# Kernel optimization log

Hardware: AMD Instinct MI355X
Metric: run time of the kernel (lower is better)

The kernel has to match this reference:

```python
import jax, jax.numpy as jnp
import numpy as np

N_NODES = 100000
N_EDGES = 1600000
B = 16
NMAX = 4096
IN_DIM = 32
H1 = 64      # capacity C
H2 = 128     # 2C
LAT = 64
DEC_H = 128  # 2C
DEC_IN = LAT + 2
FUEL = 5


def _ln(x, g, b):
    m = x.mean(-1, keepdims=True)
    v = x.var(-1, keepdims=True)
    return (x - m) / jnp.sqrt(v + 1e-5) * g + b


def _mlp2(x, wi, bi, g, be, wo, bo):
    # DeepMLP with num_layers=2: in_lin -> LayerNorm -> ReLU -> out_lin
    h = jax.nn.relu(_ln(x @ wi + bi, g, be))
    return h @ wo + bo


def setup_inputs() -> dict:
    key = jax.random.key(0)
    ks = jax.random.split(key, 48)
    d = {}
    d['x'] = jax.random.normal(ks[0], (N_NODES, IN_DIM), jnp.float32)
    d['edge_index'] = jax.random.randint(ks[1], (2, N_EDGES), 0, N_NODES)
    d['batch'] = jnp.sort(jax.random.randint(ks[2], (N_NODES,), 0, B))

    def w(k, shape):
        return (jax.random.normal(k, shape, jnp.float32) * 0.02)

    conv_shapes = {'w1m': (IN_DIM, H1), 'w2m': (H1, H2), 'w3m': (H2, LAT),
                   'w1l': (IN_DIM, H1), 'w2l': (H1, H2), 'w3l': (H2, LAT)}
    i = 3
    for nm, sh in conv_shapes.items():
        d[nm] = w(ks[i], sh); i += 1
        d['b' + nm[1:]] = jnp.zeros((sh[1],), jnp.float32)
    # node_mlp (DeepMLP dec_in->dec_h->dec_h)
    d['nm_wi'] = w(ks[i], (DEC_IN, DEC_H)); i += 1
    d['nm_bi'] = jnp.zeros((DEC_H,), jnp.float32)
    d['nm_g'] = jnp.ones((DEC_H,), jnp.float32)
    d['nm_be'] = jnp.zeros((DEC_H,), jnp.float32)
    d['nm_wo'] = w(ks[i], (DEC_H, DEC_H)); i += 1
    d['nm_bo'] = jnp.zeros((DEC_H,), jnp.float32)
    # heads
    d['ex_w'] = w(ks[i], (DEC_H, 1)); i += 1
    d['ex_b'] = jnp.zeros((1,), jnp.float32)
    d['fu_w'] = w(ks[i], (DEC_H, FUEL)); i += 1
    d['fu_b'] = jnp.zeros((FUEL,), jnp.float32)
    d['al_w'] = w(ks[i], (DEC_H, 1)); i += 1
    d['al_b'] = jnp.zeros((1,), jnp.float32)
    d['sl_w'] = w(ks[i], (DEC_H, 1)); i += 1
    d['sl_b'] = jnp.zeros((1,), jnp.float32)
    # edge_mlp (DeepMLP dec_in->dec_h->8)
    d['em_wi'] = w(ks[i], (DEC_IN, DEC_H)); i += 1
    d['em_bi'] = jnp.zeros((DEC_H,), jnp.float32)
    d['em_g'] = jnp.ones((DEC_H,), jnp.float32)
    d['em_be'] = jnp.zeros((DEC_H,), jnp.float32)
    d['em_wo'] = w(ks[i], (DEC_H, 8)); i += 1
    d['em_bo'] = jnp.zeros((8,), jnp.float32)
    d['pos_all'] = jax.random.normal(ks[i], (NMAX, 2), jnp.float32)
    return d


def reference(x, edge_index, batch,
              w1m, b1m, w2m, b2m, w3m, b3m,
              w1l, b1l, w2l, b2l, w3l, b3l,
              nm_wi, nm_bi, nm_g, nm_be, nm_wo, nm_bo,
              ex_w, ex_b, fu_w, fu_b, al_w, al_b, sl_w, sl_b,
              em_wi, em_bi, em_g, em_be, em_wo, em_bo,
              pos_all):
    # ---- GCN encoder with self-loops and symmetric normalization (PyG GCNConv) ----
    loops = jnp.arange(N_NODES)
    src = jnp.concatenate([edge_index[0], loops])
    dst = jnp.concatenate([edge_index[1], loops])
    deg = jax.ops.segment_sum(jnp.ones(src.shape, jnp.float32), dst, N_NODES)
    dinv = jax.lax.rsqrt(deg)  # deg >= 1 because of self-loops
    norm = (dinv[src] * dinv[dst])[:, None]

    def conv(h, wt, bt):
        hw = h @ wt                                   # [N, F_out]
        return jax.ops.segment_sum(norm * hw[src], dst, N_NODES) + bt

    mu = jax.nn.relu(conv(x, w1m, b1m))
    mu = jax.nn.relu(conv(mu, w2m, b2m))
    mu = jax.nn.relu(conv(mu, w3m, b3m))
    lg = jax.nn.relu(conv(x, w1l, b1l))
    lg = jax.nn.relu(conv(lg, w2l, b2l))
    lg = jax.nn.relu(conv(lg, w3l, b3l))

    cnt = jnp.maximum(jax.ops.segment_sum(jnp.ones((N_NODES,), jnp.float32), batch, B), 1.0)[:, None]
    mu_g = jax.ops.segment_sum(mu, batch, B) / cnt    # global_mean_pool [B, LAT]
    lg_g = jax.ops.segment_sum(lg, batch, B) / cnt

    z = mu_g  # eval-mode latent_sample returns mu

    # ---- decoder ----
    Z = jnp.broadcast_to(z[:, None, :], (B, NMAX, LAT))
    pos = jnp.broadcast_to(pos_all[None], (B, NMAX, 2))
    Zp = jnp.concatenate([Z, pos], -1).reshape(B * NMAX, DEC_IN)
    h = _mlp2(Zp, nm_wi, nm_bi, nm_g, nm_be, nm_wo, nm_bo)
    nodes = (h @ ex_w + ex_b).reshape(B, NMAX, 1)
    fuel = (h @ fu_w + fu_b).reshape(B, NMAX, FUEL)
    alt = (h @ al_w + al_b).reshape(B, NMAX, 1)
    slope = (h @ sl_w + sl_b).reshape(B, NMAX, 1)
    edges = _mlp2(Zp, em_wi, em_bi, em_g, em_be, em_wo, em_bo).reshape(B, NMAX, 8)
    return (nodes, edges, fuel, alt, slope, mu_g, lg_g)
```

## Files before the change

kernel.cpp:

```cpp
#include <hip/hip_runtime.h>
#include <hip/hip_bf16.h>

#define N_NODES 100000
#define N_EDGESC 1600000
#define BATCH_B 16
#define NMAXC 4096
#define LATC 64
#define CAP 64
#define NBINS 391
#define NSB 256
#define EPB ((N_EDGESC + NSB - 1) / NSB)

#define OUT_NODES 0
#define OUT_EDGES 65536
#define OUT_FUEL  589824
#define OUT_ALT   917504
#define OUT_SLOPE 983040
#define OUT_MU    1048576
#define OUT_LG    1049600

typedef float f32x2 __attribute__((ext_vector_type(2)));
typedef float f32x4 __attribute__((ext_vector_type(4)));
typedef short bf16x8 __attribute__((ext_vector_type(8)));
union U4B { uint4 u; bf16x8 b; };

__device__ __forceinline__ unsigned short f2bf(float f) {
    unsigned int u = __float_as_uint(f);
    return (unsigned short)((u + 0x7FFFu + ((u >> 16) & 1u)) >> 16);
}
__device__ __forceinline__ float bf2f(unsigned short h) {
    return __uint_as_float(((unsigned int)h) << 16);
}
__device__ __forceinline__ void f8acc(unsigned int u, float& a0, float& a1, float& a2, float& a3) {
    f32x2 lo = __builtin_amdgcn_cvt_pk_f32_fp8(u, false);
    f32x2 hi = __builtin_amdgcn_cvt_pk_f32_fp8(u, true);
    a0 += lo[0]; a1 += lo[1]; a2 += hi[0]; a3 += hi[1];
}

__global__ void batch_count(const int* __restrict__ batch, int* __restrict__ bcnt, int n) {
    int b = threadIdx.x;
    if (b >= BATCH_B) return;
    int lo = 0, hi = n;
    while (lo < hi) { int mid = (lo + hi) >> 1; if (batch[mid] < b) lo = mid + 1; else hi = mid; }
    int start = lo;
    lo = 0; hi = n;
    while (lo < hi) { int mid = (lo + hi) >> 1; if (batch[mid] <= b) lo = mid + 1; else hi = mid; }
    bcnt[b] = lo - start;
}

__global__ __launch_bounds__(1024) void histA(const int* __restrict__ dst, int* __restrict__ hist) {
    __shared__ int h[NBINS];
    int b = blockIdx.x, t = threadIdx.x;
    for (int i = t; i < NBINS; i += 1024) h[i] = 0;
    __syncthreads();
    int e0 = b * EPB, e1 = min(e0 + EPB, N_EDGESC);
    for (int i = e0 + t; i < e1; i += 1024)
        atomicAdd(&h[dst[i] >> 8], 1);
    __syncthreads();
    for (int i = t; i < NBINS; i += 1024) hist[i * NSB + b] = h[i];
}

__global__ void scanB(int* __restrict__ hist, int* __restrict__ total) {
    __shared__ int sh[NSB];
    int j = blockIdx.x, t = threadIdx.x;
    int v = hist[j * NSB + t];
    sh[t] = v; __syncthreads();
    for (int off = 1; off < NSB; off <<= 1) {
        int u = (t >= off) ? sh[t - off] : 0; __syncthreads();
        sh[t] += u; __syncthreads();
    }
    hist[j * NSB + t] = sh[t] - v;
    if (t == NSB - 1) total[j] = sh[t];
}

__global__ void scanC(const int* __restrict__ total, int* __restrict__ base) {
    __shared__ int sh[512];
    int t = threadIdx.x;
    int v = (t < NBINS) ? total[t] : 0;
    sh[t] = v; __syncthreads();
    for (int off = 1; off < 512; off <<= 1) {
        int u = (t >= off) ? sh[t - off] : 0; __syncthreads();
        sh[t] += u; __syncthreads();
    }
    if (t < NBINS) base[t] = sh[t] - v;
    if (t == NBINS - 1) base[NBINS] = sh[t];
}

__global__ __launch_bounds__(1024) void scatterD(const int* __restrict__ src, const int* __restrict__ dst,
                                                 const int* __restrict__ hist, const int* __restrict__ base,
                                                 unsigned int* __restrict__ sorted) {
    __shared__ int w0[NBINS];
    __shared__ int lc[NBINS];
    int b = blockIdx.x, t = threadIdx.x;
    for (int i = t; i < NBINS; i += 1024) {
        w0[i] = base[i] + hist[i * NSB + b];
        lc[i] = 0;
    }
    __syncthreads();
    int e0 = b * EPB, e1 = min(e0 + EPB, N_EDGESC);
    for (int i = e0 + t; i < e1; i += 1024) {
        int d = dst[i], s = src[i];
        int j = d >> 8;
        int r = atomicAdd(&lc[j], 1);
        sorted[w0[j] + r] = ((unsigned int)s << 8) | (d & 255);
    }
}

__global__ void csr_sorted(const unsigned int* __restrict__ sorted, const int* __restrict__ base,
                           int* __restrict__ adj, int* __restrict__ cnt,
                           float* __restrict__ dinv, int N) {
    __shared__ int lc[256];
    int j = blockIdx.x, t = threadIdx.x;
    lc[t] = 0; __syncthreads();
    int e0 = base[j], e1 = base[j + 1];
    int node0 = j * 256;
    for (int i = e0 + t; i < e1; i += 256) {
        unsigned int pk = sorted[i];
        int d = pk & 255;
        int r = atomicAdd(&lc[d], 1);
        if (r < CAP) adj[(size_t)(node0 + d) * CAP + r] = (int)(pk >> 8);
    }
    __syncthreads();
    int n = node0 + t;
    if (n < N) {
        int c = lc[t];
        cnt[n] = c;
        dinv[n] = rsqrtf((float)(c + 1));
    }
}

__global__ void prescale_x(const float* __restrict__ x, const float* __restrict__ dinv,
                           unsigned int* __restrict__ xs8, int total4) {
    int i4 = blockIdx.x * 256 + threadIdx.x;
    if (i4 < total4) {
        float4 v = *(const float4*)&x[i4 * 4];
        float ds = dinv[i4 >> 3] * 64.f;
        unsigned int r = 0;
        r = __builtin_amdgcn_cvt_pk_fp8_f32(v.x * ds, v.y * ds, r, false);
        r = __builtin_amdgcn_cvt_pk_fp8_f32(v.z * ds, v.w * ds, r, true);
        xs8[i4] = r;
    }
}

__global__ void agg_s32(const unsigned int* __restrict__ xs8, const int* __restrict__ cnt,
                        const int* __restrict__ adj, const float* __restrict__ dinv,
                        float* __restrict__ out, int N) {
    int t = threadIdx.x;
    int sub = t >> 3, f = t & 7;
    int n = blockIdx.x * 32 + sub;
    if (n >= N) return;
    float s0 = 0.f, s1 = 0.f, s2 = 0.f, s3 = 0.f;
    f8acc(xs8[(size_t)n * 8 + f], s0, s1, s2, s3);
    int e1 = min(cnt[n], CAP);
    const int* ap = &adj[(size_t)n * CAP];
    int e = 0;
    for (; e + 4 <= e1; e += 4) {
        int i0 = ap[e], i1 = ap[e + 1], i2 = ap[e + 2], i3 = ap[e + 3];
        unsigned int u0 = xs8[(size_t)i0 * 8 + f];
        unsigned int u1 = xs8[(size_t)i1 * 8 + f];
        unsigned int u2 = xs8[(size_t)i2 * 8 + f];
        unsigned int u3 = xs8[(size_t)i3 * 8 + f];
        f8acc(u0, s0, s1, s2, s3); f8acc(u1, s0, s1, s2, s3);
        f8acc(u2, s0, s1, s2, s3); f8acc(u3, s0, s1, s2, s3);
    }
    for (; e < e1; e++) f8acc(xs8[(size_t)ap[e] * 8 + f], s0, s1, s2, s3);
    float d = dinv[n] * (1.f / 64.f);
    *(float4*)&out[(size_t)n * 32 + f * 4] = make_float4(s0 * d, s1 * d, s2 * d, s3 * d);
}

template <bool BIASRELU, bool OUT8>
__global__ void agg128(const unsigned int* __restrict__ tbl, const int* __restrict__ cnt,
                       const int* __restrict__ adj, const float* __restrict__ dinv,
                       const float* __restrict__ bias, void* __restrict__ outv, int N) {
    int t = threadIdx.x;
    int sub = t >> 5, f = t & 31;
    int n = blockIdx.x * 8 + sub;
    if (n >= N) return;
    float s0 = 0.f, s1 = 0.f, s2 = 0.f, s3 = 0.f;
    f8acc(tbl[(size_t)n * 32 + f], s0, s1, s2, s3);
    int e1 = min(cnt[n], CAP);
    const int* ap = &adj[(size_t)n * CAP];
    int e = 0;
    for (; e + 4 <= e1; e += 4) {
        int i0 = ap[e], i1 = ap[e + 1], i2 = ap[e + 2], i3 = ap[e + 3];
        unsigned int u0 = tbl[(size_t)i0 * 32 + f];
        unsigned int u1 = tbl[(size_t)i1 * 32 + f];
        unsigned int u2 = tbl[(size_t)i2 * 32 + f];
        unsigned int u3 = tbl[(size_t)i3 * 32 + f];
        f8acc(u0, s0, s1, s2, s3); f8acc(u1, s0, s1, s2, s3);
        f8acc(u2, s0, s1, s2, s3); f8acc(u3, s0, s1, s2, s3);
    }
    for (; e < e1; e++) f8acc(tbl[(size_t)ap[e] * 32 + f], s0, s1, s2, s3);
    float d = dinv[n] * (1.f / 32.f);
    float v0 = s0 * d, v1 = s1 * d, v2 = s2 * d, v3 = s3 * d;
    if (BIASRELU) {
        float4 bv = *(const float4*)&bias[4 * f];
        v0 = fmaxf(v0 + bv.x, 0.f); v1 = fmaxf(v1 + bv.y, 0.f);
        v2 = fmaxf(v2 + bv.z, 0.f); v3 = fmaxf(v3 + bv.w, 0.f);
    }
    if (OUT8) {
        unsigned int r = 0;
        r = __builtin_amdgcn_cvt_pk_fp8_f32(v0 * 32.f, v1 * 32.f, r, false);
        r = __builtin_amdgcn_cvt_pk_fp8_f32(v2 * 32.f, v3 * 32.f, r, true);
        ((unsigned int*)outv)[(size_t)n * 32 + f] = r;
    } else {
        ushort4 u;
        u.x = f2bf(v0); u.y = f2bf(v1); u.z = f2bf(v2); u.w = f2bf(v3);
        *(ushort4*)&((unsigned short*)outv)[(size_t)n * 128 + 4 * f] = u;
    }
}

template <int K, int F>
__global__ void wprep(const float* __restrict__ Wa, const float* __restrict__ Wb,
                      unsigned int* __restrict__ wfrag) {
    constexpr int S = K / 32, C = F / 16;
    int lane = threadIdx.x;
    int bc = blockIdx.x;
    int c = bc % C;
    int s = (bc / C) % S;
    int y = bc / (C * S);
    const float* W = (y == 0) ? Wa : Wb;
    int col = c * 16 + (lane & 15);
    int k0 = s * 32 + (lane >> 4) * 8;
    unsigned int q[4];
#pragma unroll
    for (int jj = 0; jj < 4; jj++) {
        float lo = W[(size_t)(k0 + 2 * jj) * F + col];
        float hi = W[(size_t)(k0 + 2 * jj + 1) * F + col];
        q[jj] = (unsigned int)f2bf(lo) | ((unsigned int)f2bf(hi) << 16);
    }
    *(uint4*)&wfrag[((size_t)bc * 64 + lane) * 4] = make_uint4(q[0], q[1], q[2], q[3]);
}

template <int K, int F, int IN_STRIDE, int IN_OFF_Y, int OUT_STRIDE, int OUT_OFF_Y,
          bool BIASRELU, bool SCALE, int INMODE, int OUTMODE>
__global__ __launch_bounds__(256) void mfma_conv(
    const void* __restrict__ inv, const unsigned int* __restrict__ wfrag,
    const float* __restrict__ biasa, const float* __restrict__ biasb,
    const float* __restrict__ dinv, void* __restrict__ outv, int N) {
    constexpr int S = K / 32, C = F / 16;
    constexpr int FP = F + 4;
    __shared__ unsigned short buf[4][16][FP];
    int t = threadIdx.x, lane = t & 63, wave = t >> 6;
    int y = blockIdx.y;
    int n0 = blockIdx.x * 64 + wave * 16;
    const float* bias = (y == 0) ? biasa : biasb;
    const unsigned int* wf = wfrag + (size_t)y * S * C * 64 * 4;

    f32x4 acc[C];
#pragma unroll
    for (int c = 0; c < C; c++) acc[c] = (f32x4)(0.f);

    int arow = n0 + (lane & 15);
    bool aok = arow < N;
#pragma unroll
    for (int s = 0; s < S; s++) {
        U4B af; af.u = make_uint4(0u, 0u, 0u, 0u);
        if (aok) {
            if constexpr (INMODE == 2) {
                uint2 u = *(const uint2*)((const unsigned char*)inv +
                            (size_t)arow * IN_STRIDE + y * IN_OFF_Y + s * 32 + (lane >> 4) * 8);
                f32x2 p0 = __builtin_amdgcn_cvt_pk_f32_fp8(u.x, false);
                f32x2 p1 = __builtin_amdgcn_cvt_pk_f32_fp8(u.x, true);
                f32x2 p2 = __builtin_amdgcn_cvt_pk_f32_fp8(u.y, false);
                f32x2 p3 = __builtin_amdgcn_cvt_pk_f32_fp8(u.y, true);
                af.u.x = (unsigned int)f2bf(p0[0]) | ((unsigned int)f2bf(p0[1]) << 16);
                af.u.y = (unsigned int)f2bf(p1[0]) | ((unsigned int)f2bf(p1[1]) << 16);
                af.u.z = (unsigned int)f2bf(p2[0]) | ((unsigned int)f2bf(p2[1]) << 16);
                af.u.w = (unsigned int)f2bf(p3[0]) | ((unsigned int)f2bf(p3[1]) << 16);
            } else if constexpr (INMODE == 1) {
                af.u = *(const uint4*)((const unsigned short*)inv +
                            (size_t)arow * IN_STRIDE + y * IN_OFF_Y + s * 32 + (lane >> 4) * 8);
            } else {
                const float* ap = (const float*)inv + (size_t)arow * IN_STRIDE + y * IN_OFF_Y
                                  + s * 32 + (lane >> 4) * 8;
                float4 v0 = *(const float4*)ap;
                float4 v1 = *(const float4*)(ap + 4);
                af.u.x = (unsigned int)f2bf(v0.x) | ((unsigned int)f2bf(v0.y) << 16);
                af.u.y = (unsigned int)f2bf(v0.z) | ((unsigned int)f2bf(v0.w) << 16);
                af.u.z = (unsigned int)f2bf(v1.x) | ((unsigned int)f2bf(v1.y) << 16);
                af.u.w = (unsigned int)f2bf(v1.z) | ((unsigned int)f2bf(v1.w) << 16);
            }
        }
#pragma unroll
        for (int c = 0; c < C; c++) {
            U4B wb;
            wb.u = *(const uint4*)&wf[((size_t)(s * C + c) * 64 + lane) * 4];
            acc[c] = __builtin_amdgcn_mfma_f32_16x16x32_bf16(af.b, wb.b, acc[c], 0, 0, 0);
        }
    }

    constexpr float ISC = (INMODE == 2) ? (1.f / 32.f) : 1.f;
#pragma unroll
    for (int c = 0; c < C; c++) {
        int col = c * 16 + (lane & 15);
        float bv = BIASRELU ? bias[col] : 0.f;
#pragma unroll
        for (int r = 0; r < 4; r++) {
            int row = (lane >> 4) * 4 + r;
            int n = n0 + row;
            float v = acc[c][r] * ISC;
            if (BIASRELU) v = fmaxf(v + bv, 0.f);
            if (SCALE) v *= dinv[min(n, N - 1)];
            buf[wave][row][col] = f2bf(v);
        }
    }
    __syncthreads();

    constexpr int CPR = F / 8;
    for (int i = t; i < 64 * CPR; i += 256) {
        int row = i / CPR;
        int f0 = (i % CPR) * 8;
        int n = blockIdx.x * 64 + row;
        if (n >= N) continue;
        const unsigned short* bp = &buf[row >> 4][row & 15][f0];
        uint2 a = *(const uint2*)bp;
        uint2 b = *(const uint2*)(bp + 4);
        size_t off = (size_t)n * OUT_STRIDE + y * OUT_OFF_Y + f0;
        if constexpr (OUTMODE == 2) {
            float e0 = __uint_as_float(a.x << 16), e1 = __uint_as_float(a.x & 0xFFFF0000u);
            float e2 = __uint_as_float(a.y << 16), e3 = __uint_as_float(a.y & 0xFFFF0000u);
            float e4 = __uint_as_float(b.x << 16), e5 = __uint_as_float(b.x & 0xFFFF0000u);
            float e6 = __uint_as_float(b.y << 16), e7 = __uint_as_float(b.y & 0xFFFF0000u);
            unsigned int r0 = 0, r1 = 0;
            r0 = __builtin_amdgcn_cvt_pk_fp8_f32(e0 * 32.f, e1 * 32.f, r0, false);
            r0 = __builtin_amdgcn_cvt_pk_fp8_f32(e2 * 32.f, e3 * 32.f, r0, true);
            r1 = __builtin_amdgcn_cvt_pk_fp8_f32(e4 * 32.f, e5 * 32.f, r1, false);
            r1 = __builtin_amdgcn_cvt_pk_fp8_f32(e6 * 32.f, e7 * 32.f, r1, true);
            *(uint2*)((unsigned char*)outv + off) = make_uint2(r0, r1);
        } else {
            *(uint4*)((unsigned short*)outv + off) = make_uint4(a.x, a.y, b.x, b.y);
        }
    }
}

__global__ void prep_cat(const float* __restrict__ w1m, const float* __restrict__ w1l,
                         const float* __restrict__ b1m, const float* __restrict__ b1l,
                         const float* __restrict__ b3m, const float* __restrict__ b3l,
                         float* __restrict__ wcat1, float* __restrict__ bcat1,
                         float* __restrict__ bcat3) {
    int i = blockIdx.x * 256 + threadIdx.x;
    if (i < 32 * 128) {
        int k = i >> 7, f = i & 127;
        wcat1[i] = (f < 64) ? w1m[k * 64 + f] : w1l[k * 64 + f - 64];
    } else if (i < 32 * 128 + 128) {
        int f = i - 32 * 128;
        bcat1[f] = (f < 64) ? b1m[f] : b1l[f - 64];
    } else if (i < 32 * 128 + 256) {
        int f = i - 32 * 128 - 128;
        bcat3[f] = (f < 64) ? b3m[f] : b3l[f - 64];
    }
}

__global__ void prep_dec(const float* __restrict__ nm_wo, const float* __restrict__ nm_bo,
                         const float* __restrict__ ex_w, const float* __restrict__ ex_b,
                         const float* __restrict__ fu_w, const float* __restrict__ fu_b,
                         const float* __restrict__ al_w, const float* __restrict__ al_b,
                         const float* __restrict__ sl_w, const float* __restrict__ sl_b,
                         const float* __restrict__ em_wo,
                         float* __restrict__ wtn, float* __restrict__ bcn,
                         float* __restrict__ wte) {
    int idx = blockIdx.x * 256 + threadIdx.x;
    if (idx < 1024) {
        int j = idx >> 7, k = idx & 127;
        float s = 0.f;
        for (int m = 0; m < 128; m++) {
            float w = (j == 0) ? ex_w[m] : (j <= 5) ? fu_w[m * 5 + (j - 1)]
                     : (j == 6) ? al_w[m] : sl_w[m];
            s += nm_wo[k * 128 + m] * w;
        }
        wtn[j * 128 + k] = s;
    } else if (idx < 2048) {
        int i2 = idx - 1024;
        int j = i2 >> 7, k = i2 & 127;
        wte[j * 128 + k] = em_wo[k * 8 + j];
    } else if (idx < 2056) {
        int j = idx - 2048;
        float s = (j == 0) ? ex_b[0] : (j <= 5) ? fu_b[j - 1] : (j == 6) ? al_b[0] : sl_b[0];
        for (int m = 0; m < 128; m++) {
            float w = (j == 0) ? ex_w[m] : (j <= 5) ? fu_w[m * 5 + (j - 1)]
                     : (j == 6) ? al_w[m] : sl_w[m];
            s += nm_bo[m] * w;
        }
        bcn[j] = s;
    }
}

#define POOL_CHUNK 128
__global__ void pool128(const unsigned int* __restrict__ h, const int* __restrict__ batch,
                        float* __restrict__ sums, int n) {
    int f = threadIdx.x;
    int s0 = blockIdx.x * POOL_CHUNK;
    if (s0 >= n) return;
    int s1 = min(s0 + POOL_CHUNK, n);
    int cur = batch[s0];
    float a0 = 0.f, a1 = 0.f;
    for (int i = s0; i < s1; i++) {
        int b = batch[i];
        if (b != cur) {
            atomicAdd(&sums[cur * 128 + 2 * f], a0);
            atomicAdd(&sums[cur * 128 + 2 * f + 1], a1);
            a0 = a1 = 0.f; cur = b;
        }
        unsigned int u = h[(size_t)i * 64 + f];
        a0 += __uint_as_float(u << 16);
        a1 += __uint_as_float(u & 0xFFFF0000u);
    }
    atomicAdd(&sums[cur * 128 + 2 * f], a0);
    atomicAdd(&sums[cur * 128 + 2 * f + 1], a1);
}

__global__ void finalize_pool(const float* __restrict__ sums, const int* __restrict__ bcnt,
                              float* __restrict__ out, float* __restrict__ zbuf) {
    int i = blockIdx.x * 1024 + threadIdx.x;
    int b = i >> 7, f = i & 127;
    float c = fmaxf((float)bcnt[b], 1.f);
    float v = sums[i] / c;
    if (f < 64) { out[OUT_MU + b * 64 + f] = v; zbuf[b * 64 + f] = v; }
    else out[OUT_LG + b * 64 + (f - 64)] = v;
}

__global__ void zwi_kernel(const float* __restrict__ z,
                           const float* __restrict__ nm_wi, const float* __restrict__ nm_bi,
                           const float* __restrict__ em_wi, const float* __restrict__ em_bi,
                           float* __restrict__ zwi_nm, float* __restrict__ zwi_em) {
    int b = blockIdx.x, t = threadIdx.x;
    float an = nm_bi[t], ae = em_bi[t];
    for (int k = 0; k < 64; k++) {
        float zv = z[b * 64 + k];
        an += zv * nm_wi[k * 128 + t];
        ae += zv * em_wi[k * 128 + t];
    }
    zwi_nm[b * 128 + t] = an;
    zwi_em[b * 128 + t] = ae;
}

#define D3_ROWS 32

__global__ __launch_bounds__(256) void decoder3(
    const float* __restrict__ zwi_nm, const float* __restrict__ zwi_em,
    const float* __restrict__ nm_wi, const float* __restrict__ em_wi,
    const float* __restrict__ nm_g, const float* __restrict__ nm_be,
    const float* __restrict__ em_g, const float* __restrict__ em_be,
    const float* __restrict__ wtn, const float* __restrict__ bcn,
    const float* __restrict__ wte, const float* __restrict__ em_bo,
    const float* __restrict__ pos_all,
    float* __restrict__ out) {
    __shared__ float sn[D3_ROWS][132];
    __shared__ float se[D3_ROWS][132];
    __shared__ float Wn[8][132];
    __shared__ float We[8][132];
    int t = threadIdx.x;
    int lane = t & 63, wave = t >> 6;
    int rowBase = blockIdx.x * D3_ROWS;
    int b = rowBase >> 12;
    int row0 = rowBase + wave * 8;

    for (int i = t; i < 1024; i += 256) {
        Wn[i >> 7][i & 127] = wtn[i];
        We[i >> 7][i & 127] = wte[i];
    }

    int f0 = lane, f1 = lane + 64;
    float zn0 = zwi_nm[b * 128 + f0], zn1 = zwi_nm[b * 128 + f1];
    float ze0 = zwi_em[b * 128 + f0], ze1 = zwi_em[b * 128 + f1];
    float wn64_0 = nm_wi[64 * 128 + f0], wn64_1 = nm_wi[64 * 128 + f1];
    float wn65_0 = nm_wi[65 * 128 + f0], wn65_1 = nm_wi[65 * 128 + f1];
    float we64_0 = em_wi[64 * 128 + f0], we64_1 = em_wi[64 * 128 + f1];
    float we65_0 = em_wi[65 * 128 + f0], we65_1 = em_wi[65 * 128 + f1];
    float gn0 = nm_g[f0], gn1 = nm_g[f1], bn0 = nm_be[f0], bn1 = nm_be[f1];
    float ge0 = em_g[f0], ge1 = em_g[f1], be0 = em_be[f0], be1 = em_be[f1];

#pragma unroll
    for (int r = 0; r < 8; r++) {
        int row = row0 + r, i = row & (NMAXC - 1);
        float px = pos_all[i * 2], py = pos_all[i * 2 + 1];
        float a0 = zn0 + px * wn64_0 + py * wn65_0;
        float a1 = zn1 + px * wn64_1 + py * wn65_1;
        float e0 = ze0 + px * we64_0 + py * we65_0;
        float e1 = ze1 + px * we64_1 + py * we65_1;
        float sm = a0 + a1, sq = a0 * a0 + a1 * a1;
        float sme = e0 + e1, sqe = e0 * e0 + e1 * e1;
#pragma unroll
        for (int d = 1; d < 64; d <<= 1) {
            sm += __shfl_xor(sm, d); sq += __shfl_xor(sq, d);
            sme += __shfl_xor(sme, d); sqe += __shfl_xor(sqe, d);
        }
        float mean = sm * (1.f / 128.f);
        float var = sq * (1.f / 128.f) - mean * mean;
        float rstd = rsqrtf(var + 1e-5f);
        int rl = wave * 8 + r;
        sn[rl][f0] = fmaxf((a0 - mean) * rstd * gn0 + bn0, 0.f);
        sn[rl][f1] = fmaxf((a1 - mean) * rstd * gn1 + bn1, 0.f);
        float meane = sme * (1.f / 128.f);
        float vare = sqe * (1.f / 128.f) - meane * meane;
        float rstde = rsqrtf(vare + 1e-5f);
        se[rl][f0] = fmaxf((e0 - meane) * rstde * ge0 + be0, 0.f);
        se[rl][f1] = fmaxf((e1 - meane) * rstde * ge1 + be1, 0.f);
    }
    __syncthreads();

    int rl = t >> 3, j = t & 7;
    float accn = 0.f, acce = 0.f;
#pragma unroll 8
    for (int k4 = 0; k4 < 128; k4 += 4) {
        float4 sv = *(const float4*)&sn[rl][k4];
        float4 wv = *(const float4*)&Wn[j][k4];
        float4 sev = *(const float4*)&se[rl][k4];
        float4 wev = *(const float4*)&We[j][k4];
        accn += sv.x * wv.x + sv.y * wv.y + sv.z * wv.z + sv.w * wv.w;
        acce += sev.x * wev.x + sev.y * wev.y + sev.z * wev.z + sev.w * wev.w;
    }
    int row = rowBase + rl;
    accn += bcn[j];
    if (j == 0)       out[OUT_NODES + row] = accn;
    else if (j <= 5)  out[OUT_FUEL + (size_t)row * 5 + (j - 1)] = accn;
    else if (j == 6)  out[OUT_ALT + row] = accn;
    else              out[OUT_SLOPE + row] = accn;
    out[OUT_EDGES + (size_t)row * 8 + j] = acce + em_bo[j];
}

extern "C" void kernel_launch(void* const* d_in, const int* in_sizes, int n_in,
                              void* d_out, int out_size, void* d_ws, size_t ws_size,
                              hipStream_t stream) {
    const float* x    = (const float*)d_in[0];
    const int* edge   = (const int*)d_in[1];
    const int* batch  = (const int*)d_in[2];
    const float* w1m = (const float*)d_in[3];  const float* b1m = (const float*)d_in[4];
    const float* w2m = (const float*)d_in[5];  const float* b2m = (const float*)d_in[6];
    const float* w3m = (const float*)d_in[7];  const float* b3m = (const float*)d_in[8];
    const float* w1l = (const float*)d_in[9];  const float* b1l = (const float*)d_in[10];
    const float* w2l = (const float*)d_in[11]; const float* b2l = (const float*)d_in[12];
    const float* w3l = (const float*)d_in[13]; const float* b3l = (const float*)d_in[14];
    const float* nm_wi = (const float*)d_in[15]; const float* nm_bi = (const float*)d_in[16];
    const float* nm_g  = (const float*)d_in[17]; const float* nm_be = (const float*)d_in[18];
    const float* nm_wo = (const float*)d_in[19]; const float* nm_bo = (const float*)d_in[20];
    const float* ex_w = (const float*)d_in[21]; const float* ex_b = (const float*)d_in[22];
    const float* fu_w = (const float*)d_in[23]; const float* fu_b = (const float*)d_in[24];
    const float* al_w = (const float*)d_in[25]; const float* al_b = (const float*)d_in[26];
    const float* sl_w = (const float*)d_in[27]; const float* sl_b = (const float*)d_in[28];
    const float* em_wi = (const float*)d_in[29]; const float* em_bi = (const float*)d_in[30];
    const float* em_g  = (const float*)d_in[31]; const float* em_be = (const float*)d_in[32];
    const float* em_wo = (const float*)d_in[33]; const float* em_bo = (const float*)d_in[34];
    const float* pos_all = (const float*)d_in[35];
    float* out = (float*)d_out;

    char* p = (char*)d_ws;
    auto alloc = [&](size_t bytes) -> void* {
        void* r = (void*)p;
        p += ((bytes + 255) / 256) * 256;
        return r;
    };
    int* cnt      = (int*)alloc((size_t)N_NODES * 4);
    float* dinv   = (float*)alloc((size_t)N_NODES * 4);
    int* bcnt     = (int*)alloc(BATCH_B * 4);
    float* sums   = (float*)alloc(BATCH_B * 128 * 4);
    float* zbuf   = (float*)alloc(BATCH_B * LATC * 4);
    float* zwi_nm = (float*)alloc(BATCH_B * 128 * 4);
    float* zwi_em = (float*)alloc(BATCH_B * 128 * 4);
    float* wcat1  = (float*)alloc(32 * 128 * 4);
    float* bcat1  = (float*)alloc(128 * 4);
    float* bcat3  = (float*)alloc(128 * 4);
    float* wtn    = (float*)alloc(8 * 128 * 4);
    float* bcn    = (float*)alloc(8 * 4);
    float* wte    = (float*)alloc(8 * 128 * 4);
    unsigned int* wf1 = (unsigned int*)alloc((size_t)1 * 1 * 8 * 64 * 4 * 4);
    unsigned int* wf2 = (unsigned int*)alloc((size_t)2 * 2 * 8 * 64 * 4 * 4);
    unsigned int* wf3 = (unsigned int*)alloc((size_t)2 * 4 * 4 * 64 * 4 * 4);
    int* hist     = (int*)alloc((size_t)NBINS * NSB * 4);
    int* total    = (int*)alloc((size_t)NBINS * 4);
    int* base     = (int*)alloc((size_t)(NBINS + 1) * 4);
    unsigned int* sorted = (unsigned int*)alloc((size_t)N_EDGESC * 4);
    int* adj      = (int*)alloc((size_t)N_NODES * CAP * 4);
    unsigned int* xs8 = (unsigned int*)alloc((size_t)N_NODES * 8 * 4);
    float* agg0   = (float*)alloc((size_t)N_NODES * 32 * 4);
    unsigned int* hA8 = (unsigned int*)alloc((size_t)N_NODES * 32 * 4);
    unsigned int* hB8 = (unsigned int*)alloc((size_t)N_NODES * 32 * 4);
    unsigned short* h256 = (unsigned short*)alloc((size_t)N_NODES * 256 * 2);
    unsigned short* final128 = (unsigned short*)alloc((size_t)N_NODES * 128 * 2);
    unsigned int* hD8 = hA8;

    const int* srcp = edge;
    const int* dstp = edge + N_EDGESC;

    hipMemsetAsync(sums, 0, (size_t)BATCH_B * 128 * 4, stream);

    histA<<<NSB, 1024, 0, stream>>>(dstp, hist);
    scanB<<<NBINS, NSB, 0, stream>>>(hist, total);
    scanC<<<1, 512, 0, stream>>>(total, base);
    scatterD<<<NSB, 1024, 0, stream>>>(srcp, dstp, hist, base, sorted);
    csr_sorted<<<NBINS, 256, 0, stream>>>(sorted, base, adj, cnt, dinv, N_NODES);

    batch_count<<<1, 64, 0, stream>>>(batch, bcnt, N_NODES);
    prep_cat<<<17, 256, 0, stream>>>(w1m, w1l, b1m, b1l, b3m, b3l, wcat1, bcat1, bcat3);
    prep_dec<<<9, 256, 0, stream>>>(nm_wo, nm_bo, ex_w, ex_b, fu_w, fu_b, al_w, al_b,
                                    sl_w, sl_b, em_wo, wtn, bcn, wte);
    wprep<32, 128><<<1 * 1 * 8, 64, 0, stream>>>(wcat1, wcat1, wf1);
    wprep<64, 128><<<2 * 2 * 8, 64, 0, stream>>>(w2m, w2l, wf2);
    wprep<128, 64><<<2 * 4 * 4, 64, 0, stream>>>(w3m, w3l, wf3);
    prescale_x<<<(N_NODES * 8 + 255) / 256, 256, 0, stream>>>(x, dinv, xs8, N_NODES * 8);

    agg_s32<<<(N_NODES + 31) / 32, 256, 0, stream>>>(xs8, cnt, adj, dinv, agg0, N_NODES);

    const int GB = (N_NODES + 63) / 64;

    mfma_conv<32, 128, 32, 0, 128, 0, true, true, 0, 2>
        <<<dim3(GB, 1), 256, 0, stream>>>(agg0, wf1, bcat1, bcat1, dinv, hA8, N_NODES);

    agg128<false, true><<<(N_NODES + 7) / 8, 256, 0, stream>>>(
        hA8, cnt, adj, dinv, nullptr, hB8, N_NODES);

    mfma_conv<64, 128, 128, 64, 256, 128, true, false, 2, 1>
        <<<dim3(GB, 2), 256, 0, stream>>>(hB8, wf2, b2m, b2l, dinv, h256, N_NODES);

    mfma_conv<128, 64, 256, 128, 128, 64, false, true, 1, 2>
        <<<dim3(GB, 2), 256, 0, stream>>>(h256, wf3, nullptr, nullptr, dinv, hD8, N_NODES);

    agg128<true, false><<<(N_NODES + 7) / 8, 256, 0, stream>>>(
        hD8, cnt, adj, dinv, bcat3, final128, N_NODES);

    pool128<<<(N_NODES + POOL_CHUNK - 1) / POOL_CHUNK, 64, 0, stream>>>(
        (const unsigned int*)final128, batch, sums, N_NODES);
    finalize_pool<<<2, 1024, 0, stream>>>(sums, bcnt, out, zbuf);

    zwi_kernel<<<BATCH_B, 128, 0, stream>>>(zbuf, nm_wi, nm_bi, em_wi, em_bi, zwi_nm, zwi_em);

    decoder3<<<BATCH_B * NMAXC / D3_ROWS, 256, 0, stream>>>(
        zwi_nm, zwi_em, nm_wi, em_wi, nm_g, nm_be, em_g, em_be,
        wtn, bcn, wte, em_bo, pos_all, out);
}
```

Before: 311.8 us.

## Replace fixed-capacity padded adjacency with compact CSR using 4-aligned per-node offsets

The adjacency builder moves from a fixed 64-slot row per node to a compact CSR layout. Each node's segment is padded to a multiple of four and bins are spaced by a fixed pad, so the aggregation kernels can read neighbor indices with int4 loads. The gather loops are unrolled to eight neighbors per step. This shrinks the adjacency footprint from N*64 ints to roughly E ints, cutting memory traffic and improving locality, at the cost of an extra counting pass and a shared-memory scan in the CSR kernel. It also drops the silent truncation at 64 neighbors.

New measurement: 297.2 us. 4.7% less time.

```diff
diff --git a/kernel.cpp b/kernel.cpp
--- a/kernel.cpp
+++ b/kernel.cpp
@@ -6,10 +6,10 @@
 #define BATCH_B 16
 #define NMAXC 4096
 #define LATC 64
-#define CAP 64
 #define NBINS 391
 #define NSB 256
 #define EPB ((N_EDGESC + NSB - 1) / NSB)
+#define BIN_PAD 768
 
 #define OUT_NODES 0
 #define OUT_EDGES 65536
@@ -106,26 +106,41 @@
     }
 }
 
-__global__ void csr_sorted(const unsigned int* __restrict__ sorted, const int* __restrict__ base,
-                           int* __restrict__ adj, int* __restrict__ cnt,
-                           float* __restrict__ dinv, int N) {
+__global__ void csr_compact(const unsigned int* __restrict__ sorted, const int* __restrict__ base,
+                            int* __restrict__ adj, int* __restrict__ offs,
+                            int* __restrict__ cnt, float* __restrict__ dinv, int N) {
     __shared__ int lc[256];
+    __shared__ int cur[256];
+    __shared__ int so4[256];
     int j = blockIdx.x, t = threadIdx.x;
-    lc[t] = 0; __syncthreads();
+    lc[t] = 0; cur[t] = 0;
+    __syncthreads();
     int e0 = base[j], e1 = base[j + 1];
-    int node0 = j * 256;
+    for (int i = e0 + t; i < e1; i += 256)
+        atomicAdd(&lc[sorted[i] & 255], 1);
+    __syncthreads();
+    int c4 = (lc[t] + 3) & ~3;
+    so4[t] = c4;
+    __syncthreads();
+    for (int off = 1; off < 256; off <<= 1) {
+        int u = (t >= off) ? so4[t - off] : 0; __syncthreads();
+        so4[t] += u; __syncthreads();
+    }
+    int mybase = base[j] + j * BIN_PAD + so4[t] - c4;
+    __syncthreads();
+    so4[t] = mybase;
+    __syncthreads();
     for (int i = e0 + t; i < e1; i += 256) {
         unsigned int pk = sorted[i];
         int d = pk & 255;
-        int r = atomicAdd(&lc[d], 1);
-        if (r < CAP) adj[(size_t)(node0 + d) * CAP + r] = (int)(pk >> 8);
-    }
-    __syncthreads();
-    int n = node0 + t;
+        int r = atomicAdd(&cur[d], 1);
+        adj[so4[d] + r] = (int)(pk >> 8);
+    }
+    int n = j * 256 + t;
     if (n < N) {
-        int c = lc[t];
-        cnt[n] = c;
-        dinv[n] = rsqrtf((float)(c + 1));
+        cnt[n] = lc[t];
+        offs[n] = so4[t];
+        dinv[n] = rsqrtf((float)(lc[t] + 1));
     }
 }
 
@@ -143,54 +158,87 @@
 }
 
 __global__ void agg_s32(const unsigned int* __restrict__ xs8, const int* __restrict__ cnt,
-                        const int* __restrict__ adj, const float* __restrict__ dinv,
-                        float* __restrict__ out, int N) {
+                        const int* __restrict__ offs, const int* __restrict__ adj,
+                        const float* __restrict__ dinv, float* __restrict__ out, int N) {
     int t = threadIdx.x;
     int sub = t >> 3, f = t & 7;
     int n = blockIdx.x * 32 + sub;
     if (n >= N) return;
     float s0 = 0.f, s1 = 0.f, s2 = 0.f, s3 = 0.f;
     f8acc(xs8[(size_t)n * 8 + f], s0, s1, s2, s3);
-    int e1 = min(cnt[n], CAP);
-    const int* ap = &adj[(size_t)n * CAP];
-    int e = 0;
-    for (; e + 4 <= e1; e += 4) {
-        int i0 = ap[e], i1 = ap[e + 1], i2 = ap[e + 2], i3 = ap[e + 3];
-        unsigned int u0 = xs8[(size_t)i0 * 8 + f];
-        unsigned int u1 = xs8[(size_t)i1 * 8 + f];
-        unsigned int u2 = xs8[(size_t)i2 * 8 + f];
-        unsigned int u3 = xs8[(size_t)i3 * 8 + f];
+    int e = offs[n];
+    int e1 = e + cnt[n];
+    for (; e + 8 <= e1; e += 8) {
+        int4 ia = *(const int4*)&adj[e];
+        int4 ib = *(const int4*)&adj[e + 4];
+        unsigned int u0 = xs8[(size_t)ia.x * 8 + f];
+        unsigned int u1 = xs8[(size_t)ia.y * 8 + f];
+        unsigned int u2 = xs8[(size_t)ia.z * 8 + f];
+        unsigned int u3 = xs8[(size_t)ia.w * 8 + f];
+        unsigned int u4 = xs8[(size_t)ib.x * 8 + f];
+        unsigned int u5 = xs8[(size_t)ib.y * 8 + f];
+        unsigned int u6 = xs8[(size_t)ib.z * 8 + f];
+        unsigned int u7 = xs8[(size_t)ib.w * 8 + f];
         f8acc(u0, s0, s1, s2, s3); f8acc(u1, s0, s1, s2, s3);
         f8acc(u2, s0, s1, s2, s3); f8acc(u3, s0, s1, s2, s3);
-    }
-    for (; e < e1; e++) f8acc(xs8[(size_t)ap[e] * 8 + f], s0, s1, s2, s3);
+        f8acc(u4, s0, s1, s2, s3); f8acc(u5, s0, s1, s2, s3);
+        f8acc(u6, s0, s1, s2, s3); f8acc(u7, s0, s1, s2, s3);
+    }
+    if (e + 4 <= e1) {
+        int4 ia = *(const int4*)&adj[e];
+        unsigned int u0 = xs8[(size_t)ia.x * 8 + f];
+        unsigned int u1 = xs8[(size_t)ia.y * 8 + f];
+        unsigned int u2 = xs8[(size_t)ia.z * 8 + f];
+        unsigned int u3 = xs8[(size_t)ia.w * 8 + f];
+        f8acc(u0, s0, s1, s2, s3); f8acc(u1, s0, s1, s2, s3);
+        f8acc(u2, s0, s1, s2, s3); f8acc(u3, s0, s1, s2, s3);
+        e += 4;
+    }
+    for (; e < e1; e++) f8acc(xs8[(size_t)adj[e] * 8 + f], s0, s1, s2, s3);
     float d = dinv[n] * (1.f / 64.f);
     *(float4*)&out[(size_t)n * 32 + f * 4] = make_float4(s0 * d, s1 * d, s2 * d, s3 * d);
 }
 
 template <bool BIASRELU, bool OUT8>
 __global__ void agg128(const unsigned int* __restrict__ tbl, const int* __restrict__ cnt,
-                       const int* __restrict__ adj, const float* __restrict__ dinv,
-                       const float* __restrict__ bias, void* __restrict__ outv, int N) {
+                       const int* __restrict__ offs, const int* __restrict__ adj,
+                       const float* __restrict__ dinv, const float* __restrict__ bias,
+                       void* __restrict__ outv, int N) {
     int t = threadIdx.x;
     int sub = t >> 5, f = t & 31;
     int n = blockIdx.x * 8 + sub;
     if (n >= N) return;
     float s0 = 0.f, s1 = 0.f, s2 = 0.f, s3 = 0.f;
     f8acc(tbl[(size_t)n * 32 + f], s0, s1, s2, s3);
-    int e1 = min(cnt[n], CAP);
-    const int* ap = &adj[(size_t)n * CAP];
-    int e = 0;
-    for (; e + 4 <= e1; e += 4) {
-        int i0 = ap[e], i1 = ap[e + 1], i2 = ap[e + 2], i3 = ap[e + 3];
-        unsigned int u0 = tbl[(size_t)i0 * 32 + f];
-        unsigned int u1 = tbl[(size_t)i1 * 32 + f];
-        unsigned int u2 = tbl[(size_t)i2 * 32 + f];
-        unsigned int u3 = tbl[(size_t)i3 * 32 + f];
+    int e = offs[n];
+    int e1 = e + cnt[n];
+    for (; e + 8 <= e1; e += 8) {
+        int4 ia = *(const int4*)&adj[e];
+        int4 ib = *(const int4*)&adj[e + 4];
+        unsigned int u0 = tbl[(size_t)ia.x * 32 + f];
+        unsigned int u1 = tbl[(size_t)ia.y * 32 + f];
+        unsigned int u2 = tbl[(size_t)ia.z * 32 + f];
+        unsigned int u3 = tbl[(size_t)ia.w * 32 + f];
+        unsigned int u4 = tbl[(size_t)ib.x * 32 + f];
+        unsigned int u5 = tbl[(size_t)ib.y * 32 + f];
+        unsigned int u6 = tbl[(size_t)ib.z * 32 + f];
+        unsigned int u7 = tbl[(size_t)ib.w * 32 + f];
         f8acc(u0, s0, s1, s2, s3); f8acc(u1, s0, s1, s2, s3);
         f8acc(u2, s0, s1, s2, s3); f8acc(u3, s0, s1, s2, s3);
-    }
-    for (; e < e1; e++) f8acc(tbl[(size_t)ap[e] * 32 + f], s0, s1, s2, s3);
+        f8acc(u4, s0, s1, s2, s3); f8acc(u5, s0, s1, s2, s3);
+        f8acc(u6, s0, s1, s2, s3); f8acc(u7, s0, s1, s2, s3);
+    }
+    if (e + 4 <= e1) {
+        int4 ia = *(const int4*)&adj[e];
+        unsigned int u0 = tbl[(size_t)ia.x * 32 + f];
+        unsigned int u1 = tbl[(size_t)ia.y * 32 + f];
+        unsigned int u2 = tbl[(size_t)ia.z * 32 + f];
+        unsigned int u3 = tbl[(size_t)ia.w * 32 + f];
+        f8acc(u0, s0, s1, s2, s3); f8acc(u1, s0, s1, s2, s3);
+        f8acc(u2, s0, s1, s2, s3); f8acc(u3, s0, s1, s2, s3);
+        e += 4;
+    }
+    for (; e < e1; e++) f8acc(tbl[(size_t)adj[e] * 32 + f], s0, s1, s2, s3);
     float d = dinv[n] * (1.f / 32.f);
     float v0 = s0 * d, v1 = s1 * d, v2 = s2 * d, v3 = s3 * d;
     if (BIASRELU) {
@@ -552,6 +600,7 @@
         return r;
     };
     int* cnt      = (int*)alloc((size_t)N_NODES * 4);
+    int* offs     = (int*)alloc((size_t)N_NODES * 4);
     float* dinv   = (float*)alloc((size_t)N_NODES * 4);
     int* bcnt     = (int*)alloc(BATCH_B * 4);
     float* sums   = (float*)alloc(BATCH_B * 128 * 4);
@@ -571,7 +620,7 @@
     int* total    = (int*)alloc((size_t)NBINS * 4);
     int* base     = (int*)alloc((size_t)(NBINS + 1) * 4);
     unsigned int* sorted = (unsigned int*)alloc((size_t)N_EDGESC * 4);
-    int* adj      = (int*)alloc((size_t)N_NODES * CAP * 4);
+    int* adj      = (int*)alloc((size_t)(N_EDGESC + NBINS * BIN_PAD + 256) * 4);
     unsigned int* xs8 = (unsigned int*)alloc((size_t)N_NODES * 8 * 4);
     float* agg0   = (float*)alloc((size_t)N_NODES * 32 * 4);
     unsigned int* hA8 = (unsigned int*)alloc((size_t)N_NODES * 32 * 4);
@@ -589,7 +638,7 @@
     scanB<<<NBINS, NSB, 0, stream>>>(hist, total);
     scanC<<<1, 512, 0, stream>>>(total, base);
     scatterD<<<NSB, 1024, 0, stream>>>(srcp, dstp, hist, base, sorted);
-    csr_sorted<<<NBINS, 256, 0, stream>>>(sorted, base, adj, cnt, dinv, N_NODES);
+    csr_compact<<<NBINS, 256, 0, stream>>>(sorted, base, adj, offs, cnt, dinv, N_NODES);
 
     batch_count<<<1, 64, 0, stream>>>(batch, bcnt, N_NODES);
     prep_cat<<<17, 256, 0, stream>>>(w1m, w1l, b1m, b1l, b3m, b3l, wcat1, bcat1, bcat3);
@@ -600,7 +649,7 @@
     wprep<128, 64><<<2 * 4 * 4, 64, 0, stream>>>(w3m, w3l, wf3);
     prescale_x<<<(N_NODES * 8 + 255) / 256, 256, 0, stream>>>(x, dinv, xs8, N_NODES * 8);
 
-    agg_s32<<<(N_NODES + 31) / 32, 256, 0, stream>>>(xs8, cnt, adj, dinv, agg0, N_NODES);
+    agg_s32<<<(N_NODES + 31) / 32, 256, 0, stream>>>(xs8, cnt, offs, adj, dinv, agg0, N_NODES);
 
     const int GB = (N_NODES + 63) / 64;
 
@@ -608,7 +657,7 @@
         <<<dim3(GB, 1), 256, 0, stream>>>(agg0, wf1, bcat1, bcat1, dinv, hA8, N_NODES);
 
     agg128<false, true><<<(N_NODES + 7) / 8, 256, 0, stream>>>(
-        hA8, cnt, adj, dinv, nullptr, hB8, N_NODES);
+        hA8, cnt, offs, adj, dinv, nullptr, hB8, N_NODES);
 
     mfma_conv<64, 128, 128, 64, 256, 128, true, false, 2, 1>
         <<<dim3(GB, 2), 256, 0, stream>>>(hB8, wf2, b2m, b2l, dinv, h256, N_NODES);
@@ -617,7 +666,7 @@
         <<<dim3(GB, 2), 256, 0, stream>>>(h256, wf3, nullptr, nullptr, dinv, hD8, N_NODES);
 
     agg128<true, false><<<(N_NODES + 7) / 8, 256, 0, stream>>>(
-        hD8, cnt, adj, dinv, bcat3, final128, N_NODES);
+        hD8, cnt, offs, adj, dinv, bcat3, final128, N_NODES);
 
     pool128<<<(N_NODES + POOL_CHUNK - 1) / POOL_CHUNK, 64, 0, stream>>>(
         (const unsigned int*)final128, batch, sums, N_NODES);
```
